# Kernel tuning notes

Measured on AMD Instinct MI355X. Metric: run time of the kernel, lower is better.

Reference implementation:

```python
import jax, jax.numpy as jnp
import numpy as np

N_EMBED = 1024
HEAD_SIZE = 128
B, T = 8, 2048

def setup_inputs() -> dict:
    key = jax.random.key(0)
    kx, kq, kk, kv = jax.random.split(key, 4)
    x = jax.random.normal(kx, (B, T, N_EMBED), dtype=jnp.float32)
    s = N_EMBED ** -0.5
    Wq = jax.random.normal(kq, (N_EMBED, HEAD_SIZE), dtype=jnp.float32) * s
    Wk = jax.random.normal(kk, (N_EMBED, HEAD_SIZE), dtype=jnp.float32) * s
    Wv = jax.random.normal(kv, (N_EMBED, HEAD_SIZE), dtype=jnp.float32) * s
    return {"x": x, "Wq": Wq, "Wk": Wk, "Wv": Wv}

def reference(x, Wq, Wk, Wv):
    # x: [B, T, C]; single causal attention head, eval mode (dropout = identity).
    Bb, Tt, C = x.shape
    q = x @ Wq  # [B, T, H]
    k = x @ Wk  # [B, T, H]
    v = x @ Wv  # [B, T, H]
    # NOTE: original scales by C**-0.5 with C = n_embed (input dim), not head_size.
    wgt = jnp.einsum('bqh,bkh->bqk', q, k) * (C ** -0.5)  # [B, T, T]
    causal = jnp.tril(jnp.ones((Tt, Tt), dtype=bool))
    wgt = jnp.where(causal, wgt, -jnp.inf)
    wgt = jax.nn.softmax(wgt, axis=-1)
    return wgt @ v  # [B, T, H]
```

## Files before the change

### kernel.cpp

```cpp
#include <hip/hip_runtime.h>
#include <hip/hip_bf16.h>

#define B_  8
#define T_  2048
#define C_  1024
#define H_  128

using f32x4  = __attribute__((ext_vector_type(4))) float;
using bf16x8 = __attribute__((ext_vector_type(8))) short;

__device__ __forceinline__ unsigned short f2bf(float f) {
    union { float f; unsigned u; } v; v.f = f;
    unsigned r = v.u + 0x7FFFu + ((v.u >> 16) & 1u);
    return (unsigned short)(r >> 16);
}

#define GLD16(gp, lp) \
    __builtin_amdgcn_global_load_lds((const __attribute__((address_space(1))) void*)(gp), \
                                     (__attribute__((address_space(3))) void*)(lp), 16, 0, 0)

template<int C>
__device__ __forceinline__ float dppf(float v) {
    return __int_as_float(__builtin_amdgcn_update_dpp(0, __float_as_int(v), C, 0xF, 0xF, true));
}
#define DPPRED_MAX(v) { v = fmaxf(v, dppf<0xB1>(v)); v = fmaxf(v, dppf<0x4E>(v)); \
                        v = fmaxf(v, dppf<0x141>(v)); v = fmaxf(v, dppf<0x140>(v)); }
#define DPPRED_SUM(v) { v = v + dppf<0xB1>(v); v = v + dppf<0x4E>(v); \
                        v = v + dppf<0x141>(v); v = v + dppf<0x140>(v); }

__global__ void wconv_kernel(const float* __restrict__ Wq,
                             const float* __restrict__ Wk,
                             const float* __restrict__ Wv,
                             unsigned short* __restrict__ Wt) {
    int id  = blockIdx.x * 256 + threadIdx.x;
    int col = id % 384;
    int k   = id / 384;
    const float* W = (col < 128) ? Wq : ((col < 256) ? Wk : Wv);
    float v = W[k * H_ + (col & 127)];
    if (col < 128) v *= 0.03125f;
    const int kt = k >> 5, sub = (k >> 3) & 3, e = k & 7;
    const int ch = col / 192, colw = col % 192;
    Wt[(size_t)kt * 12288 + ch * 6144 + (sub * 192 + colw) * 8 + e] = f2bf(v);
}

__launch_bounds__(256, 2)
__global__ void gemm_kernel(const float* __restrict__ x,
                            const unsigned short* __restrict__ Wt,
                            unsigned short* __restrict__ qb,
                            unsigned short* __restrict__ kb,
                            unsigned short* __restrict__ vT) {
    __shared__ __align__(16) unsigned short Bs[2][6144];
    __shared__ __align__(16) unsigned short As[2][2048];

    const int tid  = threadIdx.x;
    const int wave = tid >> 6;
    const int lane = tid & 63;
    const int lo = lane & 15, hi = lane >> 4;
    const int rb = blockIdx.x >> 1;
    const int ch = blockIdx.x & 1;
    const int row0  = rb * 64;
    const int colw0 = wave * 48;

    const int arow = tid >> 2;
    const int aq   = tid & 3;
    const float* xsrc = x + (size_t)(row0 + arow) * C_ + aq * 8;

    f32x4 acc[4][3];
    #pragma unroll
    for (int rt = 0; rt < 4; ++rt)
        #pragma unroll
        for (int ct = 0; ct < 3; ++ct)
            acc[rt][ct] = f32x4{0.f, 0.f, 0.f, 0.f};

    {
        const unsigned short* g = Wt + (size_t)ch * 6144 + wave * 1536 + lane * 8;
        #pragma unroll
        for (int j = 0; j < 3; ++j)
            GLD16(g + j * 512, &Bs[0][wave * 1536 + j * 512]);
        float4 g0 = *(const float4*)(xsrc);
        float4 g1 = *(const float4*)(xsrc + 4);
        unsigned a0 = f2bf(g0.x) | ((unsigned)f2bf(g0.y) << 16);
        unsigned a1 = f2bf(g0.z) | ((unsigned)f2bf(g0.w) << 16);
        unsigned a2 = f2bf(g1.x) | ((unsigned)f2bf(g1.y) << 16);
        unsigned a3 = f2bf(g1.z) | ((unsigned)f2bf(g1.w) << 16);
        *(uint4*)&As[0][(aq * 64 + arow) * 8] = uint4{a0, a1, a2, a3};
    }
    __syncthreads();

    for (int k = 0; k < 32; ++k) {
        const int cur = k & 1;
        const int nxt = cur ^ 1;

        float4 g0, g1;
        if (k < 31) {
            const unsigned short* g = Wt + (size_t)(k + 1) * 12288 + ch * 6144
                                        + wave * 1536 + lane * 8;
            #pragma unroll
            for (int j = 0; j < 3; ++j)
                GLD16(g + j * 512, &Bs[nxt][wave * 1536 + j * 512]);
            g0 = *(const float4*)(xsrc + (k + 1) * 32);
            g1 = *(const float4*)(xsrc + (k + 1) * 32 + 4);
        }

        bf16x8 af[4], bfr[3];
        #pragma unroll
        for (int rt = 0; rt < 4; ++rt)
            af[rt] = *(const bf16x8*)&As[cur][(hi * 64 + rt * 16 + lo) * 8];
        #pragma unroll
        for (int ct = 0; ct < 3; ++ct)
            bfr[ct] = *(const bf16x8*)&Bs[cur][(hi * 192 + colw0 + ct * 16 + lo) * 8];

        __builtin_amdgcn_s_setprio(1);
        #pragma unroll
        for (int ct = 0; ct < 3; ++ct)
            #pragma unroll
            for (int rt = 0; rt < 4; ++rt)
                acc[rt][ct] = __builtin_amdgcn_mfma_f32_16x16x32_bf16(af[rt], bfr[ct], acc[rt][ct], 0, 0, 0);
        __builtin_amdgcn_s_setprio(0);

        if (k < 31) {
            unsigned a0 = f2bf(g0.x) | ((unsigned)f2bf(g0.y) << 16);
            unsigned a1 = f2bf(g0.z) | ((unsigned)f2bf(g0.w) << 16);
            unsigned a2 = f2bf(g1.x) | ((unsigned)f2bf(g1.y) << 16);
            unsigned a3 = f2bf(g1.z) | ((unsigned)f2bf(g1.w) << 16);
            *(uint4*)&As[nxt][(aq * 64 + arow) * 8] = uint4{a0, a1, a2, a3};
        }
        __syncthreads();
    }

    #pragma unroll
    for (int ct = 0; ct < 3; ++ct) {
        int col = ch * 192 + colw0 + ct * 16 + lo;
        int head = col >> 7;
        int h = col & 127;
        #pragma unroll
        for (int rt = 0; rt < 4; ++rt) {
            #pragma unroll
            for (int r = 0; r < 4; ++r) {
                int rg = row0 + rt * 16 + 4 * hi + r;
                unsigned short val = f2bf(acc[rt][ct][r]);
                if (head == 0)      qb[(size_t)rg * H_ + h] = val;
                else if (head == 1) kb[(size_t)rg * H_ + h] = val;
                else {
                    int b = rg >> 11, t = rg & (T_ - 1);
                    vT[((size_t)b * H_ + h) * T_ + t] = val;
                }
            }
        }
    }
}

__launch_bounds__(512, 2)
__global__ void attn1_kernel(const unsigned short* __restrict__ qb,
                             const unsigned short* __restrict__ kb,
                             const unsigned short* __restrict__ vT,
                             float* __restrict__ Opart,
                             float* __restrict__ MLpart) {
    __shared__ unsigned short Ks[64 * 128];
    __shared__ unsigned short Vs[128 * 64];
    __shared__ unsigned short Ps[8][16][72];

    const int tid  = threadIdx.x;
    const int wave = tid >> 6;
    const int lane = tid & 63;
    const int lo = lane & 15, hi = lane >> 4;

    const int bid   = blockIdx.x;
    const int b     = bid & 7;
    const int chunk = (bid >> 3) & 7;
    const int qt    = 7 - (bid >> 6);
    if (chunk > qt) return;

    const int kv_begin = chunk << 8;
    const size_t bT = (size_t)b * T_;
    const int qrow0 = (qt << 8) + wave * 32;

    const int krow = tid >> 3, kcol = (tid & 7) * 2;
    const int vrow = tid >> 2, vcol = (tid & 3) * 2;
    const unsigned short* kgsrc = kb + (bT + krow) * H_ + kcol * 8;
    const unsigned short* vgsrc = vT + ((size_t)b * H_ + vrow) * T_ + vcol * 8;
    unsigned short* kdst0 = &Ks[krow * 128 + ((kcol ^ (krow & 7)) * 8)];
    unsigned short* kdst1 = &Ks[krow * 128 + (((kcol + 1) ^ (krow & 7)) * 8)];
    unsigned short* vdst0 = &Vs[vrow * 64 + ((vcol ^ (vrow & 7)) * 8)];
    unsigned short* vdst1 = &Vs[vrow * 64 + (((vcol + 1) ^ (vrow & 7)) * 8)];

    bf16x8 qf[2][4];
    #pragma unroll
    for (int q2 = 0; q2 < 2; ++q2)
        #pragma unroll
        for (int kc = 0; kc < 4; ++kc)
            qf[q2][kc] = *(const bf16x8*)(qb + (bT + qrow0 + 16 * q2 + lo) * H_ + kc * 32 + 8 * hi);

    float m[2][4], l[2][4];
    f32x4 o[2][8];
    #pragma unroll
    for (int q2 = 0; q2 < 2; ++q2)
        #pragma unroll
        for (int r = 0; r < 4; ++r) { m[q2][r] = -1e30f; l[q2][r] = 0.f; }
    #pragma unroll
    for (int q2 = 0; q2 < 2; ++q2)
        #pragma unroll
        for (int ct = 0; ct < 8; ++ct) o[q2][ct] = f32x4{0.f, 0.f, 0.f, 0.f};

    uint4 kr0 = *(const uint4*)(kgsrc + (size_t)kv_begin * H_);
    uint4 kr1 = *(const uint4*)(kgsrc + (size_t)kv_begin * H_ + 8);
    uint4 vr0 = *(const uint4*)(vgsrc + kv_begin);
    uint4 vr1 = *(const uint4*)(vgsrc + kv_begin + 8);

    for (int t = 0; t < 4; ++t) {
        const int kv0 = kv_begin + t * 64;
        __syncthreads();
        *(uint4*)kdst0 = kr0;
        *(uint4*)kdst1 = kr1;
        *(uint4*)vdst0 = vr0;
        *(uint4*)vdst1 = vr1;
        __syncthreads();
        if (t < 3) {
            const int kvn = kv0 + 64;
            kr0 = *(const uint4*)(kgsrc + (size_t)kvn * H_);
            kr1 = *(const uint4*)(kgsrc + (size_t)kvn * H_ + 8);
            vr0 = *(const uint4*)(vgsrc + kvn);
            vr1 = *(const uint4*)(vgsrc + kvn + 8);
        }
        if (kv0 > qrow0 + 31) continue;

        f32x4 s[2][4];
        #pragma unroll
        for (int q2 = 0; q2 < 2; ++q2)
            #pragma unroll
            for (int ct4 = 0; ct4 < 4; ++ct4) s[q2][ct4] = f32x4{0.f, 0.f, 0.f, 0.f};
        __builtin_amdgcn_s_setprio(1);
        #pragma unroll
        for (int ct4 = 0; ct4 < 4; ++ct4) {
            const int row = ct4 * 16 + lo;
            #pragma unroll
            for (int kc = 0; kc < 4; ++kc) {
                bf16x8 kf = *(const bf16x8*)&Ks[row * 128 + (((kc * 4 + hi) ^ (row & 7)) * 8)];
                s[0][ct4] = __builtin_amdgcn_mfma_f32_16x16x32_bf16(qf[0][kc], kf, s[0][ct4], 0, 0, 0);
                s[1][ct4] = __builtin_amdgcn_mfma_f32_16x16x32_bf16(qf[1][kc], kf, s[1][ct4], 0, 0, 0);
            }
        }
        __builtin_amdgcn_s_setprio(0);

        if (kv0 + 63 >= qrow0) {
            #pragma unroll
            for (int q2 = 0; q2 < 2; ++q2)
                #pragma unroll
                for (int ct4 = 0; ct4 < 4; ++ct4)
                    #pragma unroll
                    for (int r = 0; r < 4; ++r)
                        if (kv0 + ct4 * 16 + lo > qrow0 + 16 * q2 + 4 * hi + r)
                            s[q2][ct4][r] = -1e30f;
        }

        float alpha[2][4];
        #pragma unroll
        for (int q2 = 0; q2 < 2; ++q2) {
            #pragma unroll
            for (int r = 0; r < 4; ++r) {
                float pm = fmaxf(fmaxf(s[q2][0][r], s[q2][1][r]), fmaxf(s[q2][2][r], s[q2][3][r]));
                DPPRED_MAX(pm);
                float mn = fmaxf(m[q2][r], pm);
                alpha[q2][r] = __expf(m[q2][r] - mn);
                m[q2][r] = mn;
                #pragma unroll
                for (int ct4 = 0; ct4 < 4; ++ct4) s[q2][ct4][r] = __expf(s[q2][ct4][r] - mn);
                float rs = (s[q2][0][r] + s[q2][1][r]) + (s[q2][2][r] + s[q2][3][r]);
                DPPRED_SUM(rs);
                l[q2][r] = l[q2][r] * alpha[q2][r] + rs;
            }
        }
        #pragma unroll
        for (int q2 = 0; q2 < 2; ++q2)
            #pragma unroll
            for (int ct = 0; ct < 8; ++ct)
                #pragma unroll
                for (int r = 0; r < 4; ++r) o[q2][ct][r] *= alpha[q2][r];

        bf16x8 pa[2][2];
        #pragma unroll
        for (int q2 = 0; q2 < 2; ++q2) {
            #pragma unroll
            for (int ct4 = 0; ct4 < 4; ++ct4)
                #pragma unroll
                for (int r = 0; r < 4; ++r)
                    Ps[wave][4 * hi + r][ct4 * 16 + lo] = f2bf(s[q2][ct4][r]);
            pa[q2][0] = *(const bf16x8*)&Ps[wave][lo][8 * hi];
            pa[q2][1] = *(const bf16x8*)&Ps[wave][lo][32 + 8 * hi];
        }

        __builtin_amdgcn_s_setprio(1);
        #pragma unroll
        for (int ct = 0; ct < 8; ++ct) {
            const int row = ct * 16 + lo;
            #pragma unroll
            for (int half = 0; half < 2; ++half) {
                bf16x8 vf = *(const bf16x8*)&Vs[row * 64 + (((half * 4 + hi) ^ (row & 7)) * 8)];
                o[0][ct] = __builtin_amdgcn_mfma_f32_16x16x32_bf16(pa[0][half], vf, o[0][ct], 0, 0, 0);
                o[1][ct] = __builtin_amdgcn_mfma_f32_16x16x32_bf16(pa[1][half], vf, o[1][ct], 0, 0, 0);
            }
        }
        __builtin_amdgcn_s_setprio(0);
    }

    const int slot = b * 36 + ((qt * (qt + 1)) >> 1) + chunk;
    float* op = Opart + (size_t)slot * 32768 + (size_t)(wave * 32) * 128;
    #pragma unroll
    for (int q2 = 0; q2 < 2; ++q2)
        #pragma unroll
        for (int ct = 0; ct < 8; ++ct)
            #pragma unroll
            for (int r = 0; r < 4; ++r)
                op[(16 * q2 + 4 * hi + r) * 128 + ct * 16 + lo] = o[q2][ct][r];
    if (lo == 0) {
        #pragma unroll
        for (int q2 = 0; q2 < 2; ++q2)
            #pragma unroll
            for (int r = 0; r < 4; ++r) {
                int base = slot * 512 + (wave * 32 + 16 * q2 + 4 * hi + r) * 2;
                MLpart[base]     = m[q2][r];
                MLpart[base + 1] = l[q2][r];
            }
    }
}

__launch_bounds__(128)
__global__ void attn2_kernel(const float* __restrict__ Opart,
                             const float* __restrict__ MLpart,
                             float* __restrict__ out) {
    const int bid = blockIdx.x;
    const int b   = bid & 7;
    const int qt  = (bid >> 3) & 7;
    const int sub = bid >> 6;
    const int nch = qt + 1;
    const int slot0 = b * 36 + ((qt * (qt + 1)) >> 1);

    const int tid  = threadIdx.x;
    const int row  = tid >> 2;
    const int h0   = (tid & 3) * 32;
    const int srow = sub * 32 + row;

    float M = -1e30f;
    for (int c = 0; c < nch; ++c)
        M = fmaxf(M, MLpart[(slot0 + c) * 512 + srow * 2]);
    float L = 0.f;
    for (int c = 0; c < nch; ++c) {
        float mc = MLpart[(slot0 + c) * 512 + srow * 2];
        float lc = MLpart[(slot0 + c) * 512 + srow * 2 + 1];
        L += lc * __expf(mc - M);
    }

    float4 acc[8];
    #pragma unroll
    for (int j = 0; j < 8; ++j) acc[j] = float4{0.f, 0.f, 0.f, 0.f};
    for (int c = 0; c < nch; ++c) {
        float wc = __expf(MLpart[(slot0 + c) * 512 + srow * 2] - M);
        const float4* src = (const float4*)(Opart + (size_t)(slot0 + c) * 32768 + (size_t)srow * 128 + h0);
        #pragma unroll
        for (int j = 0; j < 8; ++j) {
            float4 v = src[j];
            acc[j].x += wc * v.x; acc[j].y += wc * v.y;
            acc[j].z += wc * v.z; acc[j].w += wc * v.w;
        }
    }
    float inv = 1.f / L;
    float4* dst = (float4*)(out + ((size_t)b * T_ + qt * 256 + srow) * H_ + h0);
    #pragma unroll
    for (int j = 0; j < 8; ++j) {
        float4 v = acc[j];
        dst[j] = float4{v.x * inv, v.y * inv, v.z * inv, v.w * inv};
    }
}

extern "C" void kernel_launch(void* const* d_in, const int* in_sizes, int n_in,
                              void* d_out, int out_size, void* d_ws, size_t ws_size,
                              hipStream_t stream) {
    const float* x  = (const float*)d_in[0];
    const float* Wq = (const float*)d_in[1];
    const float* Wk = (const float*)d_in[2];
    const float* Wv = (const float*)d_in[3];
    float* out = (float*)d_out;

    char* ws = (char*)d_ws;
    unsigned short* Wt  = (unsigned short*)ws;
    unsigned short* qbf = (unsigned short*)(ws + (size_t)384 * 1024 * 2);
    unsigned short* kbf = qbf + (size_t)B_ * T_ * H_;
    unsigned short* vTf = kbf + (size_t)B_ * T_ * H_;
    float* Opart  = (float*)(vTf + (size_t)B_ * T_ * H_);
    float* MLpart = (float*)((char*)Opart + (size_t)288 * 32768 * 4);

    wconv_kernel<<<(384 * 1024) / 256, 256, 0, stream>>>(Wq, Wk, Wv, Wt);
    gemm_kernel<<<B_ * T_ / 32, 256, 0, stream>>>(x, Wt, qbf, kbf, vTf);
    attn1_kernel<<<512, 512, 0, stream>>>(qbf, kbf, vTf, Opart, MLpart);
    attn2_kernel<<<512, 128, 0, stream>>>(Opart, MLpart, out);
}
```

Measured before the change: 103.8 us.

## Compute all QKV columns per block with 512 threads and deeper x prefetch

The QKV projection GEMM now has each 512-thread block handle all 384 output columns for a 64-row tile, where before two 256-thread blocks each handled half the columns. The weight layout is changed to match. Each x row tile is now read and converted to bf16 once instead of twice, halving global x traffic. The x loads are also prefetched two k-steps ahead through a register pipeline. In exchange the block is larger, uses more LDS for the B tile, and there are half as many blocks, which can reduce occupancy or latency hiding.

```diff
diff --git a/kernel.cpp b/kernel.cpp
--- a/kernel.cpp
+++ b/kernel.cpp
@@ -39,31 +39,30 @@
     float v = W[k * H_ + (col & 127)];
     if (col < 128) v *= 0.03125f;
     const int kt = k >> 5, sub = (k >> 3) & 3, e = k & 7;
-    const int ch = col / 192, colw = col % 192;
-    Wt[(size_t)kt * 12288 + ch * 6144 + (sub * 192 + colw) * 8 + e] = f2bf(v);
-}
-
-__launch_bounds__(256, 2)
+    Wt[(size_t)kt * 12288 + (sub * 384 + col) * 8 + e] = f2bf(v);
+}
+
+__launch_bounds__(512, 2)
 __global__ void gemm_kernel(const float* __restrict__ x,
                             const unsigned short* __restrict__ Wt,
                             unsigned short* __restrict__ qb,
                             unsigned short* __restrict__ kb,
                             unsigned short* __restrict__ vT) {
-    __shared__ __align__(16) unsigned short Bs[2][6144];
+    __shared__ __align__(16) unsigned short Bs[2][12288];
     __shared__ __align__(16) unsigned short As[2][2048];
 
     const int tid  = threadIdx.x;
     const int wave = tid >> 6;
     const int lane = tid & 63;
     const int lo = lane & 15, hi = lane >> 4;
-    const int rb = blockIdx.x >> 1;
-    const int ch = blockIdx.x & 1;
-    const int row0  = rb * 64;
-    const int colw0 = wave * 48;
-
-    const int arow = tid >> 2;
-    const int aq   = tid & 3;
-    const float* xsrc = x + (size_t)(row0 + arow) * C_ + aq * 8;
+    const int row0 = blockIdx.x * 64;
+
+    const int arow = tid >> 3;
+    const int aq   = tid & 7;
+    const float* xsrc = x + (size_t)(row0 + arow) * C_ + aq * 4;
+    const int aoff = ((aq >> 1) * 64 + arow) * 8 + (aq & 1) * 4;
+
+    const unsigned short* bsrc0 = Wt + (size_t)(wave * 3) * 512 + lane * 8;
 
     f32x4 acc[4][3];
     #pragma unroll
@@ -73,34 +72,28 @@
             acc[rt][ct] = f32x4{0.f, 0.f, 0.f, 0.f};
 
     {
-        const unsigned short* g = Wt + (size_t)ch * 6144 + wave * 1536 + lane * 8;
         #pragma unroll
         for (int j = 0; j < 3; ++j)
-            GLD16(g + j * 512, &Bs[0][wave * 1536 + j * 512]);
-        float4 g0 = *(const float4*)(xsrc);
-        float4 g1 = *(const float4*)(xsrc + 4);
-        unsigned a0 = f2bf(g0.x) | ((unsigned)f2bf(g0.y) << 16);
-        unsigned a1 = f2bf(g0.z) | ((unsigned)f2bf(g0.w) << 16);
-        unsigned a2 = f2bf(g1.x) | ((unsigned)f2bf(g1.y) << 16);
-        unsigned a3 = f2bf(g1.z) | ((unsigned)f2bf(g1.w) << 16);
-        *(uint4*)&As[0][(aq * 64 + arow) * 8] = uint4{a0, a1, a2, a3};
-    }
+            GLD16(bsrc0 + j * 512, &Bs[0][(wave * 3 + j) * 512]);
+        float4 f = *(const float4*)xsrc;
+        unsigned a0 = f2bf(f.x) | ((unsigned)f2bf(f.y) << 16);
+        unsigned a1 = f2bf(f.z) | ((unsigned)f2bf(f.w) << 16);
+        *(uint2*)&As[0][aoff] = uint2{a0, a1};
+    }
+    float4 h = *(const float4*)(xsrc + 32);
     __syncthreads();
 
     for (int k = 0; k < 32; ++k) {
-        const int cur = k & 1;
-        const int nxt = cur ^ 1;
-
-        float4 g0, g1;
+        const int cur = k & 1, nxt = cur ^ 1;
+
         if (k < 31) {
-            const unsigned short* g = Wt + (size_t)(k + 1) * 12288 + ch * 6144
-                                        + wave * 1536 + lane * 8;
-            #pragma unroll
-            for (int j = 0; j < 3; ++j)
-                GLD16(g + j * 512, &Bs[nxt][wave * 1536 + j * 512]);
-            g0 = *(const float4*)(xsrc + (k + 1) * 32);
-            g1 = *(const float4*)(xsrc + (k + 1) * 32 + 4);
-        }
+            const unsigned short* g = bsrc0 + (size_t)(k + 1) * 12288;
+            GLD16(g,        &Bs[nxt][(wave * 3) * 512]);
+            GLD16(g + 512,  &Bs[nxt][(wave * 3 + 1) * 512]);
+            GLD16(g + 1024, &Bs[nxt][(wave * 3 + 2) * 512]);
+        }
+        float4 g2;
+        if (k < 30) g2 = *(const float4*)(xsrc + (k + 2) * 32);
 
         bf16x8 af[4], bfr[3];
         #pragma unroll
@@ -108,7 +101,7 @@
             af[rt] = *(const bf16x8*)&As[cur][(hi * 64 + rt * 16 + lo) * 8];
         #pragma unroll
         for (int ct = 0; ct < 3; ++ct)
-            bfr[ct] = *(const bf16x8*)&Bs[cur][(hi * 192 + colw0 + ct * 16 + lo) * 8];
+            bfr[ct] = *(const bf16x8*)&Bs[cur][(hi * 384 + wave * 48 + ct * 16 + lo) * 8];
 
         __builtin_amdgcn_s_setprio(1);
         #pragma unroll
@@ -119,31 +112,30 @@
         __builtin_amdgcn_s_setprio(0);
 
         if (k < 31) {
-            unsigned a0 = f2bf(g0.x) | ((unsigned)f2bf(g0.y) << 16);
-            unsigned a1 = f2bf(g0.z) | ((unsigned)f2bf(g0.w) << 16);
-            unsigned a2 = f2bf(g1.x) | ((unsigned)f2bf(g1.y) << 16);
-            unsigned a3 = f2bf(g1.z) | ((unsigned)f2bf(g1.w) << 16);
-            *(uint4*)&As[nxt][(aq * 64 + arow) * 8] = uint4{a0, a1, a2, a3};
+            unsigned a0 = f2bf(h.x) | ((unsigned)f2bf(h.y) << 16);
+            unsigned a1 = f2bf(h.z) | ((unsigned)f2bf(h.w) << 16);
+            *(uint2*)&As[nxt][aoff] = uint2{a0, a1};
         }
         __syncthreads();
+        h = g2;
     }
 
     #pragma unroll
     for (int ct = 0; ct < 3; ++ct) {
-        int col = ch * 192 + colw0 + ct * 16 + lo;
+        int col = wave * 48 + ct * 16 + lo;
         int head = col >> 7;
-        int h = col & 127;
+        int h2 = col & 127;
         #pragma unroll
         for (int rt = 0; rt < 4; ++rt) {
             #pragma unroll
             for (int r = 0; r < 4; ++r) {
                 int rg = row0 + rt * 16 + 4 * hi + r;
                 unsigned short val = f2bf(acc[rt][ct][r]);
-                if (head == 0)      qb[(size_t)rg * H_ + h] = val;
-                else if (head == 1) kb[(size_t)rg * H_ + h] = val;
+                if (head == 0)      qb[(size_t)rg * H_ + h2] = val;
+                else if (head == 1) kb[(size_t)rg * H_ + h2] = val;
                 else {
                     int b = rg >> 11, t = rg & (T_ - 1);
-                    vT[((size_t)b * H_ + h) * T_ + t] = val;
+                    vT[((size_t)b * H_ + h2) * T_ + t] = val;
                 }
             }
         }
@@ -390,7 +382,7 @@
     float* MLpart = (float*)((char*)Opart + (size_t)288 * 32768 * 4);
 
     wconv_kernel<<<(384 * 1024) / 256, 256, 0, stream>>>(Wq, Wk, Wv, Wt);
-    gemm_kernel<<<B_ * T_ / 32, 256, 0, stream>>>(x, Wt, qbf, kbf, vTf);
+    gemm_kernel<<<B_ * T_ / 64, 512, 0, stream>>>(x, Wt, qbf, kbf, vTf);
     attn1_kernel<<<512, 512, 0, stream>>>(qbf, kbf, vTf, Opart, MLpart);
     attn2_kernel<<<512, 128, 0, stream>>>(Opart, MLpart, out);
 }
```

Measured after the change: 92.60 us. -10.8%, faster.
